# Performance work log

Hardware: AMD Instinct MI355X
Metric: run time of the kernel (lower is better)

Reference implementation:

```python
import jax, jax.numpy as jnp
import numpy as np

NUM_HEADS = 8
HEAD_SIZE = 64
INPUT = 512
OUT = NUM_HEADS * HEAD_SIZE
B, S = 4, 2048


def setup_inputs() -> dict:
    key = jax.random.key(0)
    ks = jax.random.split(key, 6)
    return {
        "key": jax.random.normal(ks[0], (B, S, INPUT), dtype=jnp.float32),
        "key_mask": jnp.zeros((B, 1, 1, S), dtype=jnp.float32),
        "query": jax.random.normal(ks[1], (B, S, INPUT), dtype=jnp.float32),
        "value": jax.random.normal(ks[2], (B, S, INPUT), dtype=jnp.float32),
        "wq": jax.random.normal(ks[3], (INPUT, OUT), dtype=jnp.float32) * (INPUT ** -0.5),
        "wk": jax.random.normal(ks[4], (INPUT, OUT), dtype=jnp.float32) * (INPUT ** -0.5),
        "wv": jax.random.normal(ks[5], (INPUT, OUT), dtype=jnp.float32) * (INPUT ** -0.5),
    }


def _split_heads(x):
    # [B, S, H*hd] -> [B, H, S, hd]
    b, s, _ = x.shape
    return x.reshape(b, s, NUM_HEADS, HEAD_SIZE).transpose(0, 2, 1, 3)


def reference(key, key_mask, query, value, wq, wk, wv):
    q = _split_heads(query @ wq)   # [B,H,S,hd]
    k = _split_heads(key @ wk)
    v = _split_heads(value @ wv)
    scale = 1.0 / jnp.sqrt(jnp.asarray(HEAD_SIZE, q.dtype))
    logits = jnp.einsum('bhqd,bhkd->bhqk', q, k) * scale + key_mask
    attn = jax.nn.softmax(logits, axis=-1)
    out = jnp.einsum('bhqk,bhkd->bhqd', attn, v)  # [B,H,S,hd]
    out = out.transpose(0, 2, 1, 3).reshape(out.shape[0], out.shape[2], OUT)
    return out
```

## Files before the change

### kernel.cpp

```cpp
#include <hip/hip_runtime.h>

typedef _Float16 f16;
typedef f16 f16x8 __attribute__((ext_vector_type(8)));
typedef f16 f16x4 __attribute__((ext_vector_type(4)));
typedef f16 f16x2 __attribute__((ext_vector_type(2)));
typedef float f32x4 __attribute__((ext_vector_type(4)));
typedef unsigned int u32;

#define MFMA16(a, b, c) __builtin_amdgcn_mfma_f32_16x16x32_f16(a, b, c, 0, 0, 0)

#define BATCH 4
#define NHEADS 8
#define HDIM 64
#define SEQ 2048
#define DIN 512
#define DOUT 512
#define LOG2E 1.44269504f
#define C1 0.18033688f

__device__ __forceinline__ void gl_lds16(const void* g, const void* l) {
  __builtin_amdgcn_global_load_lds(
      (const __attribute__((address_space(1))) u32*)g,
      (__attribute__((address_space(3))) u32*)l, 16, 0, 0);
}

__device__ __forceinline__ float fexp2(float x) {
  float r;
  asm("v_exp_f32 %0, %1" : "=v"(r) : "v"(x));
  return r;
}

__device__ __forceinline__ f16x2 pk2(float a, float b) {
  return __builtin_bit_cast(f16x2, __builtin_amdgcn_cvt_pkrtz(a, b));
}

__device__ __forceinline__ f16x4 pk4(float a, float b, float c, float d) {
  f16x2 u0 = pk2(a, b), u1 = pk2(c, d);
  f16x4 r;
  r[0] = u0[0]; r[1] = u0[1]; r[2] = u1[0]; r[3] = u1[1];
  return r;
}

__global__ __launch_bounds__(256) void prep_w(
    const float* __restrict__ wq, const float* __restrict__ wk,
    const float* __restrict__ wv, f16* __restrict__ wT) {
  __shared__ float tile[64][65];
  const float* w = blockIdx.z == 0 ? wq : (blockIdx.z == 1 ? wk : wv);
  f16* out = wT + (size_t)blockIdx.z * DIN * DOUT;
  int k0 = blockIdx.x * 64, n0 = blockIdx.y * 64;
  int t = threadIdx.x;
  int c = t & 63, rb = t >> 6;
#pragma unroll
  for (int ph = 0; ph < 16; ++ph) {
    int r = ph * 4 + rb;
    tile[r][c] = w[(size_t)(k0 + r) * DOUT + n0 + c];
  }
  __syncthreads();
#pragma unroll
  for (int ph = 0; ph < 16; ++ph) {
    int n = ph * 4 + rb;
    out[(size_t)(n0 + n) * DIN + k0 + c] = (f16)tile[c][n];
  }
}

__global__ __launch_bounds__(256, 3) void qkv_gemm(
    const float* __restrict__ xq, const float* __restrict__ xk,
    const float* __restrict__ xv, const f16* __restrict__ wT,
    f16* __restrict__ Qo, f16* __restrict__ Ko, f16* __restrict__ Vt) {
  __shared__ __attribute__((aligned(16))) f16 smem[16384];
  f16* As = smem;
  f16* Bs = smem + 8192;
  f16* CT = smem;

  int gemm = blockIdx.z;
  const float* x = gemm == 0 ? xq : (gemm == 1 ? xk : xv);
  const f16* wt = wT + (size_t)gemm * DIN * DOUT;
  int bx = blockIdx.x;
  int m0 = (bx & 63) * 128, n0 = (bx >> 6) * 128;
  int t = threadIdx.x, w = t >> 6, lane = t & 63;
  int lr = lane & 15, lq = lane >> 4;
  int wm = (w >> 1) * 64, wn = (w & 1) * 64;

  int tr = t >> 4, tc = t & 15;
  const float* xg = x + (size_t)(m0 + tr) * DIN + tc * 4;
  int aw[8];
#pragma unroll
  for (int ph = 0; ph < 8; ++ph) {
    int r = tr + 16 * ph;
    int phys = (tc >> 1) ^ (r & 7);
    aw[ph] = r * 64 + phys * 8 + (tc & 1) * 4;
  }

  int srow = lane >> 3;
  int schunk = (lane & 7) ^ srow;
  const f16* gb[4];
  const f16* lbb[4];
#pragma unroll
  for (int j = 0; j < 4; ++j) {
    int br = w * 32 + j * 8;
    gb[j] = wt + (size_t)(n0 + br + srow) * DIN + schunk * 8;
    lbb[j] = &Bs[__builtin_amdgcn_readfirstlane(br * 64)];
  }
  int xo0 = ((0 * 4 + lq) ^ (lr & 7)) * 8;
  int xo1 = ((1 * 4 + lq) ^ (lr & 7)) * 8;

  f32x4 zero = {0.f, 0.f, 0.f, 0.f};
  f32x4 acc[4][4];
#pragma unroll
  for (int i = 0; i < 4; ++i)
#pragma unroll
    for (int j = 0; j < 4; ++j) acc[i][j] = zero;

  for (int k0 = 0; k0 < DIN; k0 += 64) {
    __syncthreads();
#pragma unroll
    for (int j = 0; j < 4; ++j) gl_lds16(gb[j] + k0, lbb[j]);
#pragma unroll
    for (int ph = 0; ph < 8; ++ph) {
      float4 a = *(const float4*)(xg + (size_t)ph * 16 * DIN + k0);
      *(f16x4*)&As[aw[ph]] = pk4(a.x, a.y, a.z, a.w);
    }
    __syncthreads();
#pragma unroll
    for (int c = 0; c < 2; ++c) {
      int xo = c ? xo1 : xo0;
      f16x8 xf[4], wf[4];
#pragma unroll
      for (int i = 0; i < 4; ++i)
        xf[i] = *(const f16x8*)&As[(wm + i * 16 + lr) * 64 + xo];
#pragma unroll
      for (int i = 0; i < 4; ++i)
        wf[i] = *(const f16x8*)&Bs[(wn + i * 16 + lr) * 64 + xo];
      if (gemm == 2) {
#pragma unroll
        for (int i = 0; i < 4; ++i)
#pragma unroll
          for (int j = 0; j < 4; ++j)
            acc[i][j] = MFMA16(xf[i], wf[j], acc[i][j]);
      } else {
#pragma unroll
        for (int i = 0; i < 4; ++i)
#pragma unroll
          for (int j = 0; j < 4; ++j)
            acc[i][j] = MFMA16(wf[i], xf[j], acc[i][j]);
      }
    }
  }

  __syncthreads();
  int b_ = m0 >> 11;
  int sl = m0 & 2047;

  if (gemm == 2) {
#pragma unroll
    for (int i = 0; i < 4; ++i) {
#pragma unroll
      for (int j = 0; j < 4; ++j) {
        int d = wn + j * 16 + lr;
        int lc = (wm >> 3) + i * 2 + (lq >> 1);
        int phys = lc ^ lr;
        *(f16x4*)&CT[d * 128 + phys * 8 + (lq & 1) * 4] =
            pk4(acc[i][j][0], acc[i][j][1], acc[i][j][2], acc[i][j][3]);
      }
    }
    __syncthreads();
    int tid16 = t & 15;
#pragma unroll
    for (int ph = 0; ph < 8; ++ph) {
      int d = ph * 16 + (t >> 4);
      int phys = tid16 ^ (d & 15);
      f16x8 vv = *(const f16x8*)&CT[d * 128 + phys * 8];
      int hgl = (n0 + d) >> 6, dd = (n0 + d) & 63;
      *(f16x8*)&Vt[(((size_t)b_ * NHEADS + hgl) * HDIM + dd) * SEQ + sl +
                   tid16 * 8] = vv;
    }
  } else {
    f16* O = gemm == 0 ? Qo : Ko;
    float sc = gemm == 0 ? C1 : 1.0f;
#pragma unroll
    for (int i = 0; i < 4; ++i) {
#pragma unroll
      for (int j = 0; j < 4; ++j) {
        int s = wm + j * 16 + lr;
        int lc = (wn >> 3) + i * 2 + (lq >> 1);
        int phys = lc ^ lr;
        *(f16x4*)&CT[s * 128 + phys * 8 + (lq & 1) * 4] =
            pk4(acc[i][j][0] * sc, acc[i][j][1] * sc, acc[i][j][2] * sc,
                acc[i][j][3] * sc);
      }
    }
    __syncthreads();
    int tid8 = t & 7;
    int hh = (t >> 3) & 1;
#pragma unroll
    for (int ph = 0; ph < 8; ++ph) {
      int s = ph * 16 + (t >> 4);
      int lc = hh * 8 + tid8;
      int phys = lc ^ (s & 15);
      f16x8 vv = *(const f16x8*)&CT[s * 128 + phys * 8];
      int hgl = (n0 >> 6) + hh;
      *(f16x8*)&O[(((size_t)b_ * NHEADS + hgl) * SEQ + sl + s) * HDIM +
                  tid8 * 8] = vv;
    }
  }
}

__global__ __launch_bounds__(256, 2) void flash_attn(
    const f16* __restrict__ Q, const f16* __restrict__ K,
    const f16* __restrict__ Vt, const float* __restrict__ mask,
    float* __restrict__ out) {
  __shared__ __attribute__((aligned(16))) f16 Ks[128 * 64];
  __shared__ __attribute__((aligned(16))) f16 Vs[64 * 128];
  __shared__ __attribute__((aligned(16))) f16 Ps[128 * 136];
  __shared__ __attribute__((aligned(16))) float Ms[SEQ];

  int bh = blockIdx.x, q0 = blockIdx.y * 128;
  int b = bh >> 3, h = bh & 7;
  int t = threadIdx.x, w = t >> 6, lane = t & 63;
  int lr = lane & 15, lq = lane >> 4;

  const f16* Qg = Q + (size_t)bh * SEQ * HDIM;
  const f16* Kg = K + (size_t)bh * SEQ * HDIM;
  const f16* Vg = Vt + (size_t)bh * HDIM * SEQ;
  const float* mg = mask + (size_t)b * SEQ;

  f16x8 qf[2][2];
#pragma unroll
  for (int u = 0; u < 2; ++u)
#pragma unroll
    for (int c = 0; c < 2; ++c)
      qf[u][c] = *(const f16x8*)(Qg +
                                 (size_t)(q0 + w * 32 + u * 16 + lr) * HDIM +
                                 c * 32 + lq * 8);

  int krow = lane >> 3;
  int kchunk = (lane & 7) ^ krow;
  const f16* gk[4];
  const f16* gv[4];
  const f16* lk[4];
  const f16* lv[4];
#pragma unroll
  for (int j = 0; j < 4; ++j) {
    int kbr = w * 32 + j * 8;
    gk[j] = Kg + (size_t)(kbr + krow) * HDIM + kchunk * 8;
    lk[j] = &Ks[__builtin_amdgcn_readfirstlane(kbr * 64)];
    int vbr = w * 16 + j * 4;
    int vchunk = (lane & 15) ^ (j * 4 + lq);
    gv[j] = Vg + (size_t)(vbr + lq) * SEQ + vchunk * 8;
    lv[j] = &Vs[__builtin_amdgcn_readfirstlane(vbr * 128)];
  }
  int xk0 = ((0 * 4 + lq) ^ (lr & 7)) * 8;
  int xk1 = ((1 * 4 + lq) ^ (lr & 7)) * 8;

  f32x4 zero = {0.f, 0.f, 0.f, 0.f};
  f32x4 acc[2][4];
#pragma unroll
  for (int u = 0; u < 2; ++u)
#pragma unroll
    for (int i = 0; i < 4; ++i) acc[u][i] = zero;
  float lsum[2] = {0.f, 0.f};

  {
    int c0 = w * 512;
    gl_lds16(mg + c0 + lane * 4, &Ms[__builtin_amdgcn_readfirstlane(c0)]);
    gl_lds16(mg + c0 + 256 + lane * 4,
             &Ms[__builtin_amdgcn_readfirstlane(c0 + 256)]);
  }
#pragma unroll
  for (int j = 0; j < 4; ++j) {
    gl_lds16(gk[j], lk[j]);
    gl_lds16(gv[j], lv[j]);
  }
  asm volatile("s_waitcnt vmcnt(0)" ::: "memory");
  __builtin_amdgcn_sched_barrier(0);
  __builtin_amdgcn_s_barrier();
  __builtin_amdgcn_sched_barrier(0);

  for (int it = 0; it < 16; ++it) {
    int k0 = it * 128;

    f32x4 s[2][8];
    __builtin_amdgcn_s_setprio(1);
#pragma unroll
    for (int nt = 0; nt < 8; ++nt) {
      f16x8 kf0 = *(const f16x8*)&Ks[(nt * 16 + lr) * 64 + xk0];
      f16x8 kf1 = *(const f16x8*)&Ks[(nt * 16 + lr) * 64 + xk1];
      s[0][nt] = MFMA16(kf0, qf[0][0], zero);
      s[0][nt] = MFMA16(kf1, qf[0][1], s[0][nt]);
      s[1][nt] = MFMA16(kf0, qf[1][0], zero);
      s[1][nt] = MFMA16(kf1, qf[1][1], s[1][nt]);
    }
    __builtin_amdgcn_s_setprio(0);

    asm volatile("s_waitcnt vmcnt(0)" ::: "memory");
    __builtin_amdgcn_sched_barrier(0);
    __builtin_amdgcn_s_barrier();
    __builtin_amdgcn_sched_barrier(0);
    if (it < 15) {
#pragma unroll
      for (int j = 0; j < 4; ++j)
        gl_lds16(gk[j] + (size_t)(k0 + 128) * HDIM, lk[j]);
    }

#pragma unroll
    for (int nt = 0; nt < 8; ++nt) {
      float4 mk = *(const float4*)&Ms[k0 + nt * 16 + lq * 4];
#pragma unroll
      for (int u = 0; u < 2; ++u) {
        float p0 = fexp2(fmaf(mk.x, LOG2E, s[u][nt][0]));
        float p1 = fexp2(fmaf(mk.y, LOG2E, s[u][nt][1]));
        float p2 = fexp2(fmaf(mk.z, LOG2E, s[u][nt][2]));
        float p3 = fexp2(fmaf(mk.w, LOG2E, s[u][nt][3]));
        lsum[u] += (p0 + p1) + (p2 + p3);
        *(f16x4*)&Ps[(w * 32 + u * 16 + lr) * 136 + nt * 16 + lq * 4] =
            pk4(p0, p1, p2, p3);
      }
    }

    __builtin_amdgcn_s_setprio(1);
#pragma unroll
    for (int ks = 0; ks < 4; ++ks) {
      f16x8 ap0 = *(const f16x8*)&Ps[(w * 32 + lr) * 136 + ks * 32 + lq * 8];
      f16x8 ap1 =
          *(const f16x8*)&Ps[(w * 32 + 16 + lr) * 136 + ks * 32 + lq * 8];
#pragma unroll
      for (int dt = 0; dt < 4; ++dt) {
        f16x8 bv = *(const f16x8*)&Vs[(dt * 16 + lr) * 128 +
                                      (((ks * 4 + lq) ^ lr) * 8)];
        acc[0][dt] = MFMA16(ap0, bv, acc[0][dt]);
        acc[1][dt] = MFMA16(ap1, bv, acc[1][dt]);
      }
    }
    __builtin_amdgcn_s_setprio(0);

    if (it < 15) {
      __builtin_amdgcn_sched_barrier(0);
      __builtin_amdgcn_s_barrier();
      __builtin_amdgcn_sched_barrier(0);
#pragma unroll
      for (int j = 0; j < 4; ++j) gl_lds16(gv[j] + k0 + 128, lv[j]);
      asm volatile("s_waitcnt vmcnt(4)" ::: "memory");
      __builtin_amdgcn_sched_barrier(0);
      __builtin_amdgcn_s_barrier();
      __builtin_amdgcn_sched_barrier(0);
    }
  }

#pragma unroll
  for (int u = 0; u < 2; ++u) {
    float l = lsum[u];
    l += __shfl_xor(l, 16);
    l += __shfl_xor(l, 32);
    float inv = 1.f / l;
    float iv[4];
#pragma unroll
    for (int r = 0; r < 4; ++r) iv[r] = __shfl(inv, lq * 4 + r);
#pragma unroll
    for (int dt = 0; dt < 4; ++dt) {
#pragma unroll
      for (int r = 0; r < 4; ++r) {
        int q = q0 + w * 32 + u * 16 + lq * 4 + r;
        int d = h * HDIM + dt * 16 + lr;
        out[((size_t)b * SEQ + q) * DOUT + d] = acc[u][dt][r] * iv[r];
      }
    }
  }
}

extern "C" void kernel_launch(void* const* d_in, const int* in_sizes, int n_in,
                              void* d_out, int out_size, void* d_ws,
                              size_t ws_size, hipStream_t stream) {
  const float* key = (const float*)d_in[0];
  const float* key_mask = (const float*)d_in[1];
  const float* query = (const float*)d_in[2];
  const float* value = (const float*)d_in[3];
  const float* wq = (const float*)d_in[4];
  const float* wk = (const float*)d_in[5];
  const float* wv = (const float*)d_in[6];
  float* out = (float*)d_out;

  char* ws = (char*)d_ws;
  f16* Qws = (f16*)(ws);
  f16* Kws = (f16*)(ws + 8388608);
  f16* Vtws = (f16*)(ws + 16777216);
  f16* wT = (f16*)(ws + 25165824);

  prep_w<<<dim3(8, 8, 3), 256, 0, stream>>>(wq, wk, wv, wT);
  qkv_gemm<<<dim3(256, 1, 3), 256, 0, stream>>>(query, key, value, wT, Qws,
                                                Kws, Vtws);
  flash_attn<<<dim3(32, 16), 256, 0, stream>>>(Qws, Kws, Vtws, key_mask, out);
}
```

Baseline: 181.9 us.

## Use 8 waves per attention block with 16 query rows each

The flash attention block grows from 256 to 512 threads, so each of 8 waves owns 16 query rows instead of 32. Each wave holds half the score and accumulator registers and issues half the K/V/mask loads, with the wait counts adjusted to match. This raises the number of waves available for latency hiding at the same LDS footprint. The cost is less register-level reuse of each K and V fragment read from LDS (two MFMAs per fragment become one) and more barrier participants.

```diff
diff --git a/kernel.cpp b/kernel.cpp
--- a/kernel.cpp
+++ b/kernel.cpp
@@ -205,7 +205,7 @@
   }
 }
 
-__global__ __launch_bounds__(256, 2) void flash_attn(
+__global__ __launch_bounds__(512, 4) void flash_attn(
     const f16* __restrict__ Q, const f16* __restrict__ K,
     const f16* __restrict__ Vt, const float* __restrict__ mask,
     float* __restrict__ out) {
@@ -224,28 +224,25 @@
   const f16* Vg = Vt + (size_t)bh * HDIM * SEQ;
   const float* mg = mask + (size_t)b * SEQ;
 
-  f16x8 qf[2][2];
-#pragma unroll
-  for (int u = 0; u < 2; ++u)
-#pragma unroll
-    for (int c = 0; c < 2; ++c)
-      qf[u][c] = *(const f16x8*)(Qg +
-                                 (size_t)(q0 + w * 32 + u * 16 + lr) * HDIM +
-                                 c * 32 + lq * 8);
+  f16x8 qf[2];
+#pragma unroll
+  for (int c = 0; c < 2; ++c)
+    qf[c] = *(const f16x8*)(Qg + (size_t)(q0 + w * 16 + lr) * HDIM + c * 32 +
+                            lq * 8);
 
   int krow = lane >> 3;
   int kchunk = (lane & 7) ^ krow;
-  const f16* gk[4];
-  const f16* gv[4];
-  const f16* lk[4];
-  const f16* lv[4];
-#pragma unroll
-  for (int j = 0; j < 4; ++j) {
-    int kbr = w * 32 + j * 8;
+  const f16* gk[2];
+  const f16* gv[2];
+  const f16* lk[2];
+  const f16* lv[2];
+#pragma unroll
+  for (int j = 0; j < 2; ++j) {
+    int kbr = w * 16 + j * 8;
     gk[j] = Kg + (size_t)(kbr + krow) * HDIM + kchunk * 8;
     lk[j] = &Ks[__builtin_amdgcn_readfirstlane(kbr * 64)];
-    int vbr = w * 16 + j * 4;
-    int vchunk = (lane & 15) ^ (j * 4 + lq);
+    int vbr = w * 8 + j * 4;
+    int vchunk = (lane & 15) ^ ((vbr + lq) & 15);
     gv[j] = Vg + (size_t)(vbr + lq) * SEQ + vchunk * 8;
     lv[j] = &Vs[__builtin_amdgcn_readfirstlane(vbr * 128)];
   }
@@ -253,21 +250,17 @@
   int xk1 = ((1 * 4 + lq) ^ (lr & 7)) * 8;
 
   f32x4 zero = {0.f, 0.f, 0.f, 0.f};
-  f32x4 acc[2][4];
-#pragma unroll
-  for (int u = 0; u < 2; ++u)
-#pragma unroll
-    for (int i = 0; i < 4; ++i) acc[u][i] = zero;
-  float lsum[2] = {0.f, 0.f};
+  f32x4 acc[4];
+#pragma unroll
+  for (int i = 0; i < 4; ++i) acc[i] = zero;
+  float lsum = 0.f;
 
   {
-    int c0 = w * 512;
+    int c0 = w * 256;
     gl_lds16(mg + c0 + lane * 4, &Ms[__builtin_amdgcn_readfirstlane(c0)]);
-    gl_lds16(mg + c0 + 256 + lane * 4,
-             &Ms[__builtin_amdgcn_readfirstlane(c0 + 256)]);
-  }
-#pragma unroll
-  for (int j = 0; j < 4; ++j) {
+  }
+#pragma unroll
+  for (int j = 0; j < 2; ++j) {
     gl_lds16(gk[j], lk[j]);
     gl_lds16(gv[j], lv[j]);
   }
@@ -279,16 +272,14 @@
   for (int it = 0; it < 16; ++it) {
     int k0 = it * 128;
 
-    f32x4 s[2][8];
+    f32x4 s[8];
     __builtin_amdgcn_s_setprio(1);
 #pragma unroll
     for (int nt = 0; nt < 8; ++nt) {
       f16x8 kf0 = *(const f16x8*)&Ks[(nt * 16 + lr) * 64 + xk0];
       f16x8 kf1 = *(const f16x8*)&Ks[(nt * 16 + lr) * 64 + xk1];
-      s[0][nt] = MFMA16(kf0, qf[0][0], zero);
-      s[0][nt] = MFMA16(kf1, qf[0][1], s[0][nt]);
-      s[1][nt] = MFMA16(kf0, qf[1][0], zero);
-      s[1][nt] = MFMA16(kf1, qf[1][1], s[1][nt]);
+      s[nt] = MFMA16(kf0, qf[0], zero);
+      s[nt] = MFMA16(kf1, qf[1], s[nt]);
     }
     __builtin_amdgcn_s_setprio(0);
 
@@ -298,37 +289,31 @@
     __builtin_amdgcn_sched_barrier(0);
     if (it < 15) {
 #pragma unroll
-      for (int j = 0; j < 4; ++j)
+      for (int j = 0; j < 2; ++j)
         gl_lds16(gk[j] + (size_t)(k0 + 128) * HDIM, lk[j]);
     }
 
 #pragma unroll
     for (int nt = 0; nt < 8; ++nt) {
       float4 mk = *(const float4*)&Ms[k0 + nt * 16 + lq * 4];
-#pragma unroll
-      for (int u = 0; u < 2; ++u) {
-        float p0 = fexp2(fmaf(mk.x, LOG2E, s[u][nt][0]));
-        float p1 = fexp2(fmaf(mk.y, LOG2E, s[u][nt][1]));
-        float p2 = fexp2(fmaf(mk.z, LOG2E, s[u][nt][2]));
-        float p3 = fexp2(fmaf(mk.w, LOG2E, s[u][nt][3]));
-        lsum[u] += (p0 + p1) + (p2 + p3);
-        *(f16x4*)&Ps[(w * 32 + u * 16 + lr) * 136 + nt * 16 + lq * 4] =
-            pk4(p0, p1, p2, p3);
-      }
+      float p0 = fexp2(fmaf(mk.x, LOG2E, s[nt][0]));
+      float p1 = fexp2(fmaf(mk.y, LOG2E, s[nt][1]));
+      float p2 = fexp2(fmaf(mk.z, LOG2E, s[nt][2]));
+      float p3 = fexp2(fmaf(mk.w, LOG2E, s[nt][3]));
+      lsum += (p0 + p1) + (p2 + p3);
+      *(f16x4*)&Ps[(w * 16 + lr) * 136 + nt * 16 + lq * 4] =
+          pk4(p0, p1, p2, p3);
     }
 
     __builtin_amdgcn_s_setprio(1);
 #pragma unroll
     for (int ks = 0; ks < 4; ++ks) {
-      f16x8 ap0 = *(const f16x8*)&Ps[(w * 32 + lr) * 136 + ks * 32 + lq * 8];
-      f16x8 ap1 =
-          *(const f16x8*)&Ps[(w * 32 + 16 + lr) * 136 + ks * 32 + lq * 8];
+      f16x8 ap = *(const f16x8*)&Ps[(w * 16 + lr) * 136 + ks * 32 + lq * 8];
 #pragma unroll
       for (int dt = 0; dt < 4; ++dt) {
         f16x8 bv = *(const f16x8*)&Vs[(dt * 16 + lr) * 128 +
                                       (((ks * 4 + lq) ^ lr) * 8)];
-        acc[0][dt] = MFMA16(ap0, bv, acc[0][dt]);
-        acc[1][dt] = MFMA16(ap1, bv, acc[1][dt]);
+        acc[dt] = MFMA16(ap, bv, acc[dt]);
       }
     }
     __builtin_amdgcn_s_setprio(0);
@@ -338,17 +323,16 @@
       __builtin_amdgcn_s_barrier();
       __builtin_amdgcn_sched_barrier(0);
 #pragma unroll
-      for (int j = 0; j < 4; ++j) gl_lds16(gv[j] + k0 + 128, lv[j]);
-      asm volatile("s_waitcnt vmcnt(4)" ::: "memory");
+      for (int j = 0; j < 2; ++j) gl_lds16(gv[j] + k0 + 128, lv[j]);
+      asm volatile("s_waitcnt vmcnt(2)" ::: "memory");
       __builtin_amdgcn_sched_barrier(0);
       __builtin_amdgcn_s_barrier();
       __builtin_amdgcn_sched_barrier(0);
     }
   }
 
-#pragma unroll
-  for (int u = 0; u < 2; ++u) {
-    float l = lsum[u];
+  {
+    float l = lsum;
     l += __shfl_xor(l, 16);
     l += __shfl_xor(l, 32);
     float inv = 1.f / l;
@@ -359,9 +343,9 @@
     for (int dt = 0; dt < 4; ++dt) {
 #pragma unroll
       for (int r = 0; r < 4; ++r) {
-        int q = q0 + w * 32 + u * 16 + lq * 4 + r;
+        int q = q0 + w * 16 + lq * 4 + r;
         int d = h * HDIM + dt * 16 + lr;
-        out[((size_t)b * SEQ + q) * DOUT + d] = acc[u][dt][r] * iv[r];
+        out[((size_t)b * SEQ + q) * DOUT + d] = acc[dt][r] * iv[r];
       }
     }
   }
@@ -388,5 +372,5 @@
   prep_w<<<dim3(8, 8, 3), 256, 0, stream>>>(wq, wk, wv, wT);
   qkv_gemm<<<dim3(256, 1, 3), 256, 0, stream>>>(query, key, value, wT, Qws,
                                                 Kws, Vtws);
-  flash_attn<<<dim3(32, 16), 256, 0, stream>>>(Qws, Kws, Vtws, key_mask, out);
-}
+  flash_attn<<<dim3(32, 16), 512, 0, stream>>>(Qws, Kws, Vtws, key_mask, out);
+}
```

Measured after the change: 185.0 us. Within noise of the previous version (+1.7%).

## Switch attention to 32x32 MFMA and keep P in registers via permlane swaps

Applied to the files above, without the earlier changes.

Rewrites the flash-attention inner loop to use 32x32x16 f16 MFMA for both QK^T and PV instead of 16x16x32. The softmax probabilities are no longer staged through the Ps shared-memory buffer. They are packed to f16 and rearranged across wave halves with permlane32_swap to form the A operand directly. This removes an LDS write/read round trip per tile and frees about 34 KB of LDS. The V swizzle and the output/normalisation mapping are adjusted to the 32x32 accumulator layout, and the final 1/l values are shared through the mask buffer.

```diff
diff --git a/kernel.cpp b/kernel.cpp
--- a/kernel.cpp
+++ b/kernel.cpp
@@ -5,9 +5,13 @@
 typedef f16 f16x4 __attribute__((ext_vector_type(4)));
 typedef f16 f16x2 __attribute__((ext_vector_type(2)));
 typedef float f32x4 __attribute__((ext_vector_type(4)));
+typedef float f32x16 __attribute__((ext_vector_type(16)));
 typedef unsigned int u32;
+typedef u32 u32x2 __attribute__((ext_vector_type(2)));
+typedef u32 u32x4 __attribute__((ext_vector_type(4)));
 
 #define MFMA16(a, b, c) __builtin_amdgcn_mfma_f32_16x16x32_f16(a, b, c, 0, 0, 0)
+#define MFMA32(a, b, c) __builtin_amdgcn_mfma_f32_32x32x16_f16(a, b, c, 0, 0, 0)
 
 #define BATCH 4
 #define NHEADS 8
@@ -28,6 +32,10 @@
   float r;
   asm("v_exp_f32 %0, %1" : "=v"(r) : "v"(x));
   return r;
+}
+
+__device__ __forceinline__ u32 pk2u(float a, float b) {
+  return __builtin_bit_cast(u32, __builtin_amdgcn_cvt_pkrtz(a, b));
 }
 
 __device__ __forceinline__ f16x2 pk2(float a, float b) {
@@ -211,27 +219,18 @@
     float* __restrict__ out) {
   __shared__ __attribute__((aligned(16))) f16 Ks[128 * 64];
   __shared__ __attribute__((aligned(16))) f16 Vs[64 * 128];
-  __shared__ __attribute__((aligned(16))) f16 Ps[128 * 136];
   __shared__ __attribute__((aligned(16))) float Ms[SEQ];
 
   int bh = blockIdx.x, q0 = blockIdx.y * 128;
   int b = bh >> 3, h = bh & 7;
   int t = threadIdx.x, w = t >> 6, lane = t & 63;
   int lr = lane & 15, lq = lane >> 4;
+  int l5 = lane & 31, hf = lane >> 5;
 
   const f16* Qg = Q + (size_t)bh * SEQ * HDIM;
   const f16* Kg = K + (size_t)bh * SEQ * HDIM;
   const f16* Vg = Vt + (size_t)bh * HDIM * SEQ;
   const float* mg = mask + (size_t)b * SEQ;
-
-  f16x8 qf[2][2];
-#pragma unroll
-  for (int u = 0; u < 2; ++u)
-#pragma unroll
-    for (int c = 0; c < 2; ++c)
-      qf[u][c] = *(const f16x8*)(Qg +
-                                 (size_t)(q0 + w * 32 + u * 16 + lr) * HDIM +
-                                 c * 32 + lq * 8);
 
   int krow = lane >> 3;
   int kchunk = (lane & 7) ^ krow;
@@ -245,20 +244,10 @@
     gk[j] = Kg + (size_t)(kbr + krow) * HDIM + kchunk * 8;
     lk[j] = &Ks[__builtin_amdgcn_readfirstlane(kbr * 64)];
     int vbr = w * 16 + j * 4;
-    int vchunk = (lane & 15) ^ (j * 4 + lq);
+    int vchunk = (lane & 15) ^ ((vbr + lq) & 15);
     gv[j] = Vg + (size_t)(vbr + lq) * SEQ + vchunk * 8;
     lv[j] = &Vs[__builtin_amdgcn_readfirstlane(vbr * 128)];
   }
-  int xk0 = ((0 * 4 + lq) ^ (lr & 7)) * 8;
-  int xk1 = ((1 * 4 + lq) ^ (lr & 7)) * 8;
-
-  f32x4 zero = {0.f, 0.f, 0.f, 0.f};
-  f32x4 acc[2][4];
-#pragma unroll
-  for (int u = 0; u < 2; ++u)
-#pragma unroll
-    for (int i = 0; i < 4; ++i) acc[u][i] = zero;
-  float lsum[2] = {0.f, 0.f};
 
   {
     int c0 = w * 512;
@@ -271,6 +260,20 @@
     gl_lds16(gk[j], lk[j]);
     gl_lds16(gv[j], lv[j]);
   }
+
+  f16x8 qf[4];
+#pragma unroll
+  for (int ds = 0; ds < 4; ++ds)
+    qf[ds] = *(const f16x8*)(Qg + (size_t)(q0 + w * 32 + l5) * HDIM + ds * 16 +
+                             hf * 8);
+
+  f32x16 acc[2];
+#pragma unroll
+  for (int dt = 0; dt < 2; ++dt)
+#pragma unroll
+    for (int i = 0; i < 16; ++i) acc[dt][i] = 0.f;
+  float lsum = 0.f;
+
   asm volatile("s_waitcnt vmcnt(0)" ::: "memory");
   __builtin_amdgcn_sched_barrier(0);
   __builtin_amdgcn_s_barrier();
@@ -278,19 +281,32 @@
 
   for (int it = 0; it < 16; ++it) {
     int k0 = it * 128;
-
-    f32x4 s[2][8];
-    __builtin_amdgcn_s_setprio(1);
-#pragma unroll
-    for (int nt = 0; nt < 8; ++nt) {
-      f16x8 kf0 = *(const f16x8*)&Ks[(nt * 16 + lr) * 64 + xk0];
-      f16x8 kf1 = *(const f16x8*)&Ks[(nt * 16 + lr) * 64 + xk1];
-      s[0][nt] = MFMA16(kf0, qf[0][0], zero);
-      s[0][nt] = MFMA16(kf1, qf[0][1], s[0][nt]);
-      s[1][nt] = MFMA16(kf0, qf[1][0], zero);
-      s[1][nt] = MFMA16(kf1, qf[1][1], s[1][nt]);
-    }
-    __builtin_amdgcn_s_setprio(0);
+    u32 pk_[4][4][2];
+
+#pragma unroll
+    for (int nt = 0; nt < 4; ++nt) {
+      f32x16 s = {0.f, 0.f, 0.f, 0.f, 0.f, 0.f, 0.f, 0.f,
+                  0.f, 0.f, 0.f, 0.f, 0.f, 0.f, 0.f, 0.f};
+      __builtin_amdgcn_s_setprio(1);
+#pragma unroll
+      for (int ds = 0; ds < 4; ++ds) {
+        f16x8 kf = *(const f16x8*)&Ks[(nt * 32 + l5) * 64 +
+                                      (((ds * 2 + hf) ^ (l5 & 7)) * 8)];
+        s = MFMA32(kf, qf[ds], s);
+      }
+      __builtin_amdgcn_s_setprio(0);
+#pragma unroll
+      for (int run = 0; run < 4; ++run) {
+        float4 mk = *(const float4*)&Ms[k0 + nt * 32 + run * 8 + 4 * hf];
+        float p0 = fexp2(fmaf(mk.x, LOG2E, s[run * 4 + 0]));
+        float p1 = fexp2(fmaf(mk.y, LOG2E, s[run * 4 + 1]));
+        float p2 = fexp2(fmaf(mk.z, LOG2E, s[run * 4 + 2]));
+        float p3 = fexp2(fmaf(mk.w, LOG2E, s[run * 4 + 3]));
+        lsum += (p0 + p1) + (p2 + p3);
+        pk_[nt][run][0] = pk2u(p0, p1);
+        pk_[nt][run][1] = pk2u(p2, p3);
+      }
+    }
 
     asm volatile("s_waitcnt vmcnt(0)" ::: "memory");
     __builtin_amdgcn_sched_barrier(0);
@@ -302,33 +318,23 @@
         gl_lds16(gk[j] + (size_t)(k0 + 128) * HDIM, lk[j]);
     }
 
-#pragma unroll
-    for (int nt = 0; nt < 8; ++nt) {
-      float4 mk = *(const float4*)&Ms[k0 + nt * 16 + lq * 4];
-#pragma unroll
-      for (int u = 0; u < 2; ++u) {
-        float p0 = fexp2(fmaf(mk.x, LOG2E, s[u][nt][0]));
-        float p1 = fexp2(fmaf(mk.y, LOG2E, s[u][nt][1]));
-        float p2 = fexp2(fmaf(mk.z, LOG2E, s[u][nt][2]));
-        float p3 = fexp2(fmaf(mk.w, LOG2E, s[u][nt][3]));
-        lsum[u] += (p0 + p1) + (p2 + p3);
-        *(f16x4*)&Ps[(w * 32 + u * 16 + lr) * 136 + nt * 16 + lq * 4] =
-            pk4(p0, p1, p2, p3);
-      }
-    }
-
     __builtin_amdgcn_s_setprio(1);
 #pragma unroll
-    for (int ks = 0; ks < 4; ++ks) {
-      f16x8 ap0 = *(const f16x8*)&Ps[(w * 32 + lr) * 136 + ks * 32 + lq * 8];
-      f16x8 ap1 =
-          *(const f16x8*)&Ps[(w * 32 + 16 + lr) * 136 + ks * 32 + lq * 8];
-#pragma unroll
-      for (int dt = 0; dt < 4; ++dt) {
-        f16x8 bv = *(const f16x8*)&Vs[(dt * 16 + lr) * 128 +
-                                      (((ks * 4 + lq) ^ lr) * 8)];
-        acc[0][dt] = MFMA16(ap0, bv, acc[0][dt]);
-        acc[1][dt] = MFMA16(ap1, bv, acc[1][dt]);
+    for (int ks = 0; ks < 8; ++ks) {
+      const int nt = ks >> 1;
+      const int ge = 2 * (ks & 1);
+      const int go = 2 * (ks & 1) + 1;
+      u32x2 r0 = __builtin_amdgcn_permlane32_swap(pk_[nt][ge][0],
+                                                  pk_[nt][go][0], false, false);
+      u32x2 r1 = __builtin_amdgcn_permlane32_swap(pk_[nt][ge][1],
+                                                  pk_[nt][go][1], false, false);
+      u32x4 apw = {r0[0], r1[0], r0[1], r1[1]};
+      f16x8 ap = __builtin_bit_cast(f16x8, apw);
+#pragma unroll
+      for (int dt = 0; dt < 2; ++dt) {
+        f16x8 bv = *(const f16x8*)&Vs[(dt * 32 + l5) * 128 +
+                                      (((ks * 2 + hf) ^ (l5 & 15)) * 8)];
+        acc[dt] = MFMA32(ap, bv, acc[dt]);
       }
     }
     __builtin_amdgcn_s_setprio(0);
@@ -346,23 +352,23 @@
     }
   }
 
-#pragma unroll
-  for (int u = 0; u < 2; ++u) {
-    float l = lsum[u];
-    l += __shfl_xor(l, 16);
-    l += __shfl_xor(l, 32);
-    float inv = 1.f / l;
-    float iv[4];
-#pragma unroll
-    for (int r = 0; r < 4; ++r) iv[r] = __shfl(inv, lq * 4 + r);
-#pragma unroll
-    for (int dt = 0; dt < 4; ++dt) {
-#pragma unroll
-      for (int r = 0; r < 4; ++r) {
-        int q = q0 + w * 32 + u * 16 + lq * 4 + r;
-        int d = h * HDIM + dt * 16 + lr;
-        out[((size_t)b * SEQ + q) * DOUT + d] = acc[u][dt][r] * iv[r];
-      }
+  float l = lsum + __shfl_xor(lsum, 32);
+  float inv = 1.f / l;
+  Ms[w * 32 + l5] = inv;
+  asm volatile("s_waitcnt lgkmcnt(0)" ::: "memory");
+  __builtin_amdgcn_sched_barrier(0);
+  float ivq[16];
+#pragma unroll
+  for (int r = 0; r < 16; ++r)
+    ivq[r] = Ms[w * 32 + (r & 3) + 8 * (r >> 2) + 4 * hf];
+
+#pragma unroll
+  for (int dt = 0; dt < 2; ++dt) {
+#pragma unroll
+    for (int r = 0; r < 16; ++r) {
+      int q = q0 + w * 32 + (r & 3) + 8 * (r >> 2) + 4 * hf;
+      int d = h * HDIM + dt * 32 + l5;
+      out[((size_t)b * SEQ + q) * DOUT + d] = acc[dt][r] * ivq[r];
     }
   }
 }
```

Result: no change. 182.6 us (+0.4%).
